# Kernel tuning notes

Hardware: AMD Instinct MI355X
Metric: run time of the kernel (lower is better)

Reference implementation:

```python
import jax, jax.numpy as jnp
import numpy as np

B, T, D = 2, 2048, 2048
Q_HEADS, KV_HEADS, HEAD_DIM = 16, 4, 128
ROPE_BASE = 10000.0


def _apply_rotary(x_nhd, positions_n):
    # x_nhd: (N, H, head_dim); half-split rotary embedding.
    half = x_nhd.shape[-1] // 2
    inv_freq = 1.0 / (ROPE_BASE ** (jnp.arange(half, dtype=jnp.float32) / half))
    ang = positions_n.astype(jnp.float32)[:, None] * inv_freq  # (N, half)
    cos = jnp.cos(ang)[:, None, :]  # (N, 1, half)
    sin = jnp.sin(ang)[:, None, :]
    x1, x2 = x_nhd[..., :half], x_nhd[..., half:]
    return jnp.concatenate([x1 * cos - x2 * sin, x1 * sin + x2 * cos], axis=-1)


def setup_inputs() -> dict:
    key = jax.random.key(0)
    ks = jax.random.split(key, 5)
    s_in = 1.0 / np.sqrt(D)
    s_o = 1.0 / np.sqrt(Q_HEADS * HEAD_DIM)
    x = jax.random.normal(ks[0], (B, T, D), dtype=jnp.float32)
    positions = jnp.broadcast_to(jnp.arange(T, dtype=jnp.int32), (B, T))
    wq = jax.random.normal(ks[1], (Q_HEADS * HEAD_DIM, D), dtype=jnp.float32) * s_in
    wk = jax.random.normal(ks[2], (KV_HEADS * HEAD_DIM, D), dtype=jnp.float32) * s_in
    wv = jax.random.normal(ks[3], (KV_HEADS * HEAD_DIM, D), dtype=jnp.float32) * s_in
    wo = jax.random.normal(ks[4], (D, Q_HEADS * HEAD_DIM), dtype=jnp.float32) * s_o
    return {"x": x, "positions": positions, "wq": wq, "wk": wk, "wv": wv, "wo": wo}


def reference(x, positions, wq, wk, wv, wo):
    bsz, tsz, _ = x.shape
    q = jnp.einsum('btd,od->bto', x, wq).reshape(bsz, tsz, Q_HEADS, HEAD_DIM)
    k = jnp.einsum('btd,od->bto', x, wk).reshape(bsz, tsz, KV_HEADS, HEAD_DIM)
    v = jnp.einsum('btd,od->bto', x, wv).reshape(bsz, tsz, KV_HEADS, HEAD_DIM)
    pos_flat = positions.reshape(-1)
    q = _apply_rotary(q.reshape(-1, Q_HEADS, HEAD_DIM), pos_flat).reshape(bsz, tsz, Q_HEADS, HEAD_DIM)
    k = _apply_rotary(k.reshape(-1, KV_HEADS, HEAD_DIM), pos_flat).reshape(bsz, tsz, KV_HEADS, HEAD_DIM)
    rep = Q_HEADS // KV_HEADS
    k = jnp.repeat(k, rep, axis=2)
    v = jnp.repeat(v, rep, axis=2)
    logits = jnp.einsum('bthd,bThd->bhtT', q, k) / jnp.sqrt(jnp.float32(HEAD_DIM))
    causal = jnp.tril(jnp.ones((tsz, tsz), dtype=bool))
    logits = jnp.where(causal[None, None], logits, -1e9)
    weights = jax.nn.softmax(logits, axis=-1)
    ctx = jnp.einsum('bhtT,bThd->bthd', weights, v).reshape(bsz, tsz, Q_HEADS * HEAD_DIM)
    return jnp.einsum('bto,do->btd', ctx, wo)
```

## Files before the change

### kernel.cpp

```cpp
#include <hip/hip_runtime.h>
#include <hip/hip_bf16.h>

typedef __bf16 bf16x8 __attribute__((ext_vector_type(8)));
typedef float  f32x4  __attribute__((ext_vector_type(4)));
typedef float  f32x16 __attribute__((ext_vector_type(16)));
typedef unsigned int u32x2 __attribute__((ext_vector_type(2)));

#define B_   2
#define T_   2048
#define D_   2048
#define QH_  16
#define KVH_ 4
#define HD_  128
#define BT_  (B_ * T_)
#define KVD_ 512
#define SCL  0.12751744f
#define NIF  -0.20762050593f

#define GLOAD_LDS16(g, l)                                        \
  __builtin_amdgcn_global_load_lds(                              \
      (const __attribute__((address_space(1))) void*)(g),        \
      (__attribute__((address_space(3))) void*)(l), 16, 0, 0)

#define SWZ(row)  ((((row) >> 3) ^ (row)) & 15)
#define SWZ8(row) ((((row) >> 3) ^ (row)) & 7)
#define SWZ4(row) (((row) >> 1) & 3)

__global__ __launch_bounds__(256) void cvt_all(
    const float* __restrict__ x, const float* __restrict__ wq,
    const float* __restrict__ wk, const float* __restrict__ wv,
    const float* __restrict__ wo, ushort* __restrict__ out) {
  const int i = blockIdx.x * 256 + threadIdx.x;
  int j = i;
  const float* src;
  float mul = 1.f;
  if (j < 2097152) { src = x; }
  else if ((j -= 2097152) < 1048576) { src = wq; mul = SCL; }
  else if ((j -= 1048576) < 262144)  { src = wk; }
  else if ((j -= 262144) < 262144)   { src = wv; }
  else { j -= 262144; src = wo; }
  float4 v = ((const float4*)src)[j];
  __hip_bfloat16 h0 = __float2bfloat16(v.x * mul);
  __hip_bfloat16 h1 = __float2bfloat16(v.y * mul);
  __hip_bfloat16 h2 = __float2bfloat16(v.z * mul);
  __hip_bfloat16 h3 = __float2bfloat16(v.w * mul);
  ushort4 o;
  o.x = *(ushort*)&h0; o.y = *(ushort*)&h1;
  o.z = *(ushort*)&h2; o.w = *(ushort*)&h3;
  ((ushort4*)out)[i] = o;
}

__global__ __launch_bounds__(256, 2) void gemm_qkv(
    const ushort* __restrict__ X, const ushort* __restrict__ WQ,
    const ushort* __restrict__ WK, const ushort* __restrict__ WV,
    const int* __restrict__ positions,
    ushort* __restrict__ qo, ushort* __restrict__ ko, ushort* __restrict__ vo) {
  const int nb = blockIdx.x % 24;
  const int mb = blockIdx.x / 24;
  const int tid = threadIdx.x;
  const int wave = tid >> 6;
  const int lane = tid & 63;
  const int mrow = lane & 15;
  const int quad = lane >> 4;
  const int wm = wave >> 1;
  const int wn = wave & 1;
  const int m0 = mb * 128;
  const int K = D_;

  const ushort* Wg;
  if (nb < 16)      Wg = WQ + (size_t)nb * 128 * K;
  else if (nb < 20) Wg = WK + (size_t)(nb - 16) * 128 * K;
  else              Wg = WV + (size_t)(nb - 20) * 128 * K;

  __shared__ __align__(16) ushort smem[16640];
  ushort* Atp = smem;
  ushort* Btp = smem + 8192;

  f32x4 acc[4][4];
#pragma unroll
  for (int i = 0; i < 4; ++i)
#pragma unroll
    for (int j = 0; j < 4; ++j) acc[i][j] = (f32x4){0.f, 0.f, 0.f, 0.f};

  const ushort* Xg = X + (size_t)m0 * K;

  auto STAGE = [&](int buf, int k0) {
#pragma unroll
    for (int p = 0; p < 2; ++p) {
      const int c = p * 256 + tid;
      const int row = c >> 2;
      const int cc = (c & 3) ^ SWZ4(row);
      GLOAD_LDS16(Xg + (size_t)row * K + k0 + cc * 8,
                  Atp + (size_t)buf * 4096 + (size_t)(p * 256 + wave * 64) * 8);
      GLOAD_LDS16(Wg + (size_t)row * K + k0 + cc * 8,
                  Btp + (size_t)buf * 4096 + (size_t)(p * 256 + wave * 64) * 8);
    }
  };

  const int NT = K / 32;
  STAGE(0, 0);
  STAGE(1, 32);

  for (int t = 0; t < NT; ++t) {
    const int cur = t & 1;
    if (t + 2 < NT) asm volatile("s_waitcnt vmcnt(4)" ::: "memory");
    else            asm volatile("s_waitcnt vmcnt(0)" ::: "memory");
    __builtin_amdgcn_s_barrier();

    const ushort* Ac = Atp + (size_t)cur * 4096;
    const ushort* Bc = Btp + (size_t)cur * 4096;
    bf16x8 af[4], bfr[4];
#pragma unroll
    for (int mt = 0; mt < 4; ++mt) {
      const int row = wm * 64 + mt * 16 + mrow;
      af[mt] = *reinterpret_cast<const bf16x8*>(
          Ac + row * 32 + ((quad ^ SWZ4(row)) * 8));
    }
#pragma unroll
    for (int nt = 0; nt < 4; ++nt) {
      const int row = wn * 64 + nt * 16 + mrow;
      bfr[nt] = *reinterpret_cast<const bf16x8*>(
          Bc + row * 32 + ((quad ^ SWZ4(row)) * 8));
    }
#pragma unroll
    for (int mt = 0; mt < 4; ++mt)
#pragma unroll
      for (int nt = 0; nt < 4; ++nt)
        acc[mt][nt] = __builtin_amdgcn_mfma_f32_16x16x32_bf16(
            af[mt], bfr[nt], acc[mt][nt], 0, 0, 0);

    asm volatile("s_waitcnt lgkmcnt(0)" ::: "memory");
    __builtin_amdgcn_s_barrier();
    if (t + 2 < NT) STAGE(cur, (t + 2) * 32);
  }

  if (nb < 20) {
    float* sC = (float*)smem;
    ushort* outp; int ldo, colbase;
    if (nb < 16) { outp = qo; ldo = 2048; colbase = nb * 128; }
    else         { outp = ko; ldo = KVD_; colbase = (nb - 16) * 128; }

    const int col = tid & 63;
    const int wv = tid >> 6;
    const float inv = exp2f((float)col * NIF);

#pragma unroll
    for (int rh = 0; rh < 2; ++rh) {
      if (wm == rh) {
#pragma unroll
        for (int mt = 0; mt < 4; ++mt)
#pragma unroll
          for (int nt = 0; nt < 4; ++nt) {
            const int colw = wn * 64 + nt * 16 + mrow;
            const int r0 = mt * 16 + quad * 4;
#pragma unroll
            for (int r = 0; r < 4; ++r)
              sC[(r0 + r) * 130 + colw] = acc[mt][nt][r];
          }
      }
      __syncthreads();
#pragma unroll 4
      for (int i = 0; i < 16; ++i) {
        const int rl = i * 4 + wv;
        const int grow = m0 + rh * 64 + rl;
        const float x1 = sC[rl * 130 + col];
        const float x2 = sC[rl * 130 + col + 64];
        const float pos = (float)positions[grow];
        const float ang = pos * inv;
        const float cc = cosf(ang);
        const float ss = sinf(ang);
        __hip_bfloat16 h1 = __float2bfloat16(x1 * cc - x2 * ss);
        __hip_bfloat16 h2 = __float2bfloat16(x1 * ss + x2 * cc);
        outp[(size_t)grow * ldo + colbase + col] = *(ushort*)&h1;
        outp[(size_t)grow * ldo + colbase + col + 64] = *(ushort*)&h2;
      }
      __syncthreads();
    }
  } else {
#pragma unroll
    for (int mt = 0; mt < 4; ++mt) {
#pragma unroll
      for (int nt = 0; nt < 4; ++nt) {
        const int colw = wn * 64 + nt * 16 + mrow;
        const int row0 = m0 + wm * 64 + mt * 16 + quad * 4;
        const int col = (nb - 20) * 128 + colw;
        const int bb = row0 >> 11;
        const int t0 = row0 & (T_ - 1);
        ushort4 s4;
#pragma unroll
        for (int r = 0; r < 4; ++r) {
          __hip_bfloat16 hh = __float2bfloat16(acc[mt][nt][r]);
          (&s4.x)[r] = *(ushort*)&hh;
        }
        *(ushort4*)(vo + ((size_t)(bb * KVD_ + col)) * T_ + t0) = s4;
      }
    }
  }
}

__global__ __launch_bounds__(256) void gemm_o(
    const ushort* __restrict__ X, const ushort* __restrict__ W,
    float* __restrict__ Y, int M, int N, int K) {
  const int nb128 = N >> 7;
  const int mb = blockIdx.x / nb128;
  const int nb = blockIdx.x % nb128;
  const int tid = threadIdx.x;
  const int wave = tid >> 6;
  const int lane = tid & 63;
  const int mrow = lane & 15;
  const int quad = lane >> 4;
  const int wm = wave >> 1;
  const int wn = wave & 1;
  const int m0 = mb * 128;
  const int n0 = nb * 128;

  __shared__ __align__(16) ushort At[2][128 * 64];
  __shared__ __align__(16) ushort Bt[2][128 * 64];

  f32x4 acc[4][4];
#pragma unroll
  for (int i = 0; i < 4; ++i)
#pragma unroll
    for (int j = 0; j < 4; ++j) acc[i][j] = (f32x4){0.f, 0.f, 0.f, 0.f};

  const ushort* Xg = X + (size_t)m0 * K;
  const ushort* Wg = W + (size_t)n0 * K;

  auto STAGE = [&](int buf, int k0) {
#pragma unroll
    for (int p = 0; p < 4; ++p) {
      const int c = p * 256 + tid;
      const int row = c >> 3;
      const int cc = (c & 7) ^ (row & 7);
      GLOAD_LDS16(Xg + (size_t)row * K + k0 + cc * 8,
                  At[buf] + (size_t)(p * 256 + wave * 64) * 8);
      GLOAD_LDS16(Wg + (size_t)row * K + k0 + cc * 8,
                  Bt[buf] + (size_t)(p * 256 + wave * 64) * 8);
    }
  };

  const int NT = K / 64;
  STAGE(0, 0);
  STAGE(1, 64);

  for (int t = 0; t < NT; ++t) {
    const int cur = t & 1;
    if (t + 2 < NT) asm volatile("s_waitcnt vmcnt(8)" ::: "memory");
    else            asm volatile("s_waitcnt vmcnt(0)" ::: "memory");
    __builtin_amdgcn_s_barrier();

    const ushort* Ac = At[cur];
    const ushort* Bc = Bt[cur];
#pragma unroll
    for (int s = 0; s < 2; ++s) {
      bf16x8 af[4], bfr[4];
#pragma unroll
      for (int mt = 0; mt < 4; ++mt) {
        const int row = wm * 64 + mt * 16 + mrow;
        af[mt] = *reinterpret_cast<const bf16x8*>(
            Ac + row * 64 + (((s * 4 + quad) ^ (row & 7)) * 8));
      }
#pragma unroll
      for (int nt = 0; nt < 4; ++nt) {
        const int row = wn * 64 + nt * 16 + mrow;
        bfr[nt] = *reinterpret_cast<const bf16x8*>(
            Bc + row * 64 + (((s * 4 + quad) ^ (row & 7)) * 8));
      }
#pragma unroll
      for (int mt = 0; mt < 4; ++mt)
#pragma unroll
        for (int nt = 0; nt < 4; ++nt)
          acc[mt][nt] = __builtin_amdgcn_mfma_f32_16x16x32_bf16(
              af[mt], bfr[nt], acc[mt][nt], 0, 0, 0);
    }

    asm volatile("s_waitcnt lgkmcnt(0)" ::: "memory");
    __builtin_amdgcn_s_barrier();
    if (t + 2 < NT) STAGE(cur, (t + 2) * 64);
  }

#pragma unroll
  for (int mt = 0; mt < 4; ++mt)
#pragma unroll
    for (int nt = 0; nt < 4; ++nt) {
      const int col = n0 + wn * 64 + nt * 16 + mrow;
      const int row0 = m0 + wm * 64 + mt * 16 + quad * 4;
#pragma unroll
      for (int r = 0; r < 4; ++r)
        Y[(size_t)(row0 + r) * N + col] = acc[mt][nt][r];
    }
}

static __device__ __forceinline__ unsigned pk2(float a, float b) {
  __hip_bfloat16 ha = __float2bfloat16(a);
  __hip_bfloat16 hb = __float2bfloat16(b);
  return (unsigned)(*(ushort*)&ha) | ((unsigned)(*(ushort*)&hb) << 16);
}

static __device__ __forceinline__ void hswap(unsigned& a, unsigned& b,
                                             const int hi) {
#if __has_builtin(__builtin_amdgcn_permlane32_swap)
  u32x2 r = __builtin_amdgcn_permlane32_swap(a, b, false, false);
  a = r.x;
  b = r.y;
#else
  unsigned s = __shfl_xor(hi ? a : b, 32, 64);
  unsigned na = hi ? s : a;
  b = hi ? b : s;
  a = na;
#endif
}

__global__ __launch_bounds__(256, 2) void attn_mfma(
    const ushort* __restrict__ q, const ushort* __restrict__ k,
    const ushort* __restrict__ vt, ushort* __restrict__ ctx) {
  const int tid = threadIdx.x;
  const int wave = tid >> 6;
  const int lane = tid & 63;
  const int m5 = lane & 31;
  const int hi = lane >> 5;
  const int parity = wave & 1;
  const int hh = wave >> 1;

  const int pj = blockIdx.x & 31;
  const int g  = blockIdx.x >> 5;
  const int b   = g >> 3;
  const int hkv = (g >> 1) & 3;
  const int hp  = g & 1;
  const int hq  = hkv * 4 + hp * 2 + hh;

  __shared__ __align__(16) ushort smem[32768];
  __shared__ float lbuf[2][32];

  const ushort* kbase = k + ((size_t)b * T_ * KVH_ + hkv) * HD_;
  const ushort* vbase = vt + (size_t)(b * KVD_ + hkv * HD_) * T_;

  for (int job = 0; job < 2; ++job) {
    const int qt = job ? pj : 63 - pj;
    const int q0 = qt * 32;
    const int ns = (qt >> 1) + 1;

    const ushort* qrow =
        q + ((size_t)(b * T_ + q0 + m5) * QH_ + hq) * HD_ + hi * 8;
    bf16x8 qf[8];
#pragma unroll
    for (int c = 0; c < 8; ++c)
      qf[c] = *reinterpret_cast<const bf16x8*>(qrow + c * 16);

    f32x16 o4[4];
#pragma unroll
    for (int dt = 0; dt < 4; ++dt)
#pragma unroll
      for (int r = 0; r < 16; ++r) o4[dt][r] = 0.f;
    float ls = 0.f;

    auto STAGE = [&](int buf, int s) {
      const int j0 = s * 64;
      ushort* kb_ = smem + buf * 16384;
      ushort* vb_ = smem + buf * 16384 + 8192;
#pragma unroll
      for (int p = 0; p < 4; ++p) {
        const int c = p * 256 + tid;
        const int krow = c >> 4;
        const int kco = (c & 15) ^ SWZ(krow);
        GLOAD_LDS16(kbase + (size_t)(j0 + krow) * KVD_ + kco * 8,
                    kb_ + (size_t)(p * 256 + wave * 64) * 8);
      }
#pragma unroll
      for (int p = 0; p < 4; ++p) {
        const int c = p * 256 + tid;
        const int vrow = c >> 3;
        const int vco = (c & 7) ^ SWZ8(vrow);
        GLOAD_LDS16(vbase + (size_t)vrow * T_ + j0 + vco * 8,
                    vb_ + (size_t)(p * 256 + wave * 64) * 8);
      }
    };

    STAGE(0, 0);

    for (int s = 0; s < ns; ++s) {
      const int cur = s & 1;
      if (s + 1 < ns) {
        STAGE(cur ^ 1, s + 1);
        asm volatile("s_waitcnt vmcnt(8)" ::: "memory");
      } else {
        asm volatile("s_waitcnt vmcnt(0)" ::: "memory");
      }
      __builtin_amdgcn_s_barrier();

      const ushort* kt  = smem + cur * 16384;
      const ushort* vtl = smem + cur * 16384 + 8192;
      const int c32 = 2 * s + parity;

      if (c32 <= qt) {
        __builtin_amdgcn_s_setprio(1);
        f32x16 sa;
#pragma unroll
        for (int r = 0; r < 16; ++r) sa[r] = 0.f;
        const int rowk = parity * 32 + m5;
#pragma unroll
        for (int c = 0; c < 8; ++c) {
          const int ch = (2 * c + hi) ^ SWZ(rowk);
          bf16x8 kf =
              *reinterpret_cast<const bf16x8*>(kt + rowk * 128 + ch * 8);
          sa = __builtin_amdgcn_mfma_f32_32x32x16_bf16(kf, qf[c], sa, 0, 0, 0);
        }

        float p[16];
        if (c32 == qt) {
#pragma unroll
          for (int r = 0; r < 16; ++r) {
            const int roff = (r & 3) + 8 * (r >> 2) + 4 * hi;
            p[r] = (roff > m5) ? 0.f : exp2f(sa[r]);
          }
        } else {
#pragma unroll
          for (int r = 0; r < 16; ++r) p[r] = exp2f(sa[r]);
        }
#pragma unroll
        for (int r = 0; r < 16; ++r) ls += p[r];

        unsigned u0 = pk2(p[0], p[1]);   unsigned u1 = pk2(p[2], p[3]);
        unsigned u2 = pk2(p[4], p[5]);   unsigned u3 = pk2(p[6], p[7]);
        unsigned u4 = pk2(p[8], p[9]);   unsigned u5 = pk2(p[10], p[11]);
        unsigned u6 = pk2(p[12], p[13]); unsigned u7 = pk2(p[14], p[15]);
        hswap(u0, u2, hi); hswap(u1, u3, hi);
        hswap(u4, u6, hi); hswap(u5, u7, hi);

#pragma unroll
        for (int half = 0; half < 2; ++half) {
          union { unsigned w[4]; bf16x8 v; } pa;
          pa.w[0] = half ? u4 : u0;
          pa.w[1] = half ? u5 : u1;
          pa.w[2] = half ? u6 : u2;
          pa.w[3] = half ? u7 : u3;
          const int gc2 = parity * 4 + half * 2;
#pragma unroll
          for (int dt = 0; dt < 4; ++dt) {
            const int rowv = dt * 32 + m5;
            const int chv = (gc2 + hi) ^ SWZ8(rowv);
            bf16x8 vf =
                *reinterpret_cast<const bf16x8*>(vtl + rowv * 64 + chv * 8);
            o4[dt] = __builtin_amdgcn_mfma_f32_32x32x16_bf16(pa.v, vf, o4[dt],
                                                             0, 0, 0);
          }
        }
        __builtin_amdgcn_s_setprio(0);
      }

      asm volatile("s_waitcnt lgkmcnt(0)" ::: "memory");
      __builtin_amdgcn_s_barrier();
    }

    const float lt = ls + __shfl_xor(ls, 32, 64);
    float* sO = (float*)smem;
    if (parity) {
#pragma unroll
      for (int reg = 0; reg < 16; ++reg) {
        const int qrw = (reg & 3) + 8 * (reg >> 2) + 4 * hi;
#pragma unroll
        for (int dt = 0; dt < 4; ++dt)
          sO[hh * 4096 + qrw * 128 + dt * 32 + m5] = o4[dt][reg];
      }
      if (hi == 0) lbuf[hh][m5] = lt;
    }
    __syncthreads();
    if (!parity) {
      const float ltot = lt + lbuf[hh][m5];
#pragma unroll
      for (int reg = 0; reg < 16; ++reg) {
        const int qrw = (reg & 3) + 8 * (reg >> 2) + 4 * hi;
        const float rl = 1.f / __shfl(ltot, qrw, 64);
        ushort* op =
            ctx + ((size_t)(b * T_ + q0 + qrw) * QH_ + hq) * HD_ + m5;
#pragma unroll
        for (int dt = 0; dt < 4; ++dt) {
          const float ov =
              o4[dt][reg] + sO[hh * 4096 + qrw * 128 + dt * 32 + m5];
          __hip_bfloat16 hb = __float2bfloat16(ov * rl);
          op[dt * 32] = *(ushort*)&hb;
        }
      }
    }
    __syncthreads();
  }
}

extern "C" void kernel_launch(void* const* d_in, const int* in_sizes, int n_in,
                              void* d_out, int out_size, void* d_ws, size_t ws_size,
                              hipStream_t stream) {
  const float* x  = (const float*)d_in[0];
  const int* pos  = (const int*)d_in[1];
  const float* wq = (const float*)d_in[2];
  const float* wk = (const float*)d_in[3];
  const float* wv = (const float*)d_in[4];
  const float* wo = (const float*)d_in[5];

  ushort* xb  = (ushort*)d_ws;
  ushort* wqb = xb  + (size_t)8388608;
  ushort* wkb = wqb + (size_t)4194304;
  ushort* wvb = wkb + (size_t)1048576;
  ushort* wob = wvb + (size_t)1048576;
  ushort* qb  = wob + (size_t)4194304;
  ushort* kb  = qb  + (size_t)8388608;
  ushort* vtb = kb  + (size_t)2097152;
  ushort* ctx = xb;

  cvt_all<<<18432, 256, 0, stream>>>(x, wq, wk, wv, wo, (ushort*)d_ws);

  gemm_qkv<<<(BT_ / 128) * 24, 256, 0, stream>>>(
      xb, wqb, wkb, wvb, pos, qb, kb, vtb);

  attn_mfma<<<512, 256, 0, stream>>>(qb, kb, vtb, ctx);

  gemm_o<<<(BT_ / 128) * (D_ / 128), 256, 0, stream>>>(
      ctx, wob, (float*)d_out, BT_, D_, QH_ * HD_);
}
```

Baseline: 290.0 us.

## Deepen QKV GEMM K-tile to 64 with single-buffered A and remap gemm_o blocks

The QKV projection GEMM now stages 64-wide K slices with an 8-way XOR swizzle, halving the number of barrier-separated main-loop iterations. X tiles are single-buffered while weight tiles stay double-buffered, and the vmcnt accounting is adjusted to match. The min-blocks launch bound is dropped and LDS grows to 48KB, which may lower occupancy. gemm_o blocks are remapped so that consecutive block IDs spread row tiles across groups of eight, aiming at better L2 locality per XCD; this mapping hard-codes the 32x16 tile grid.

```diff
diff --git a/kernel.cpp b/kernel.cpp
--- a/kernel.cpp
+++ b/kernel.cpp
@@ -24,7 +24,6 @@
 
 #define SWZ(row)  ((((row) >> 3) ^ (row)) & 15)
 #define SWZ8(row) ((((row) >> 3) ^ (row)) & 7)
-#define SWZ4(row) (((row) >> 1) & 3)
 
 __global__ __launch_bounds__(256) void cvt_all(
     const float* __restrict__ x, const float* __restrict__ wq,
@@ -50,7 +49,7 @@
   ((ushort4*)out)[i] = o;
 }
 
-__global__ __launch_bounds__(256, 2) void gemm_qkv(
+__global__ __launch_bounds__(256) void gemm_qkv(
     const ushort* __restrict__ X, const ushort* __restrict__ WQ,
     const ushort* __restrict__ WK, const ushort* __restrict__ WV,
     const int* __restrict__ positions,
@@ -72,9 +71,9 @@
   else if (nb < 20) Wg = WK + (size_t)(nb - 16) * 128 * K;
   else              Wg = WV + (size_t)(nb - 20) * 128 * K;
 
-  __shared__ __align__(16) ushort smem[16640];
-  ushort* Atp = smem;
-  ushort* Btp = smem + 8192;
+  __shared__ __align__(16) ushort smem[24576];
+  ushort* Ab = smem;
+  ushort* Bb = smem + 8192;
 
   f32x4 acc[4][4];
 #pragma unroll
@@ -84,54 +83,67 @@
 
   const ushort* Xg = X + (size_t)m0 * K;
 
-  auto STAGE = [&](int buf, int k0) {
-#pragma unroll
-    for (int p = 0; p < 2; ++p) {
+  auto STAGE_A = [&](int k0) {
+#pragma unroll
+    for (int p = 0; p < 4; ++p) {
       const int c = p * 256 + tid;
-      const int row = c >> 2;
-      const int cc = (c & 3) ^ SWZ4(row);
+      const int row = c >> 3;
+      const int cc = (c & 7) ^ (row & 7);
       GLOAD_LDS16(Xg + (size_t)row * K + k0 + cc * 8,
-                  Atp + (size_t)buf * 4096 + (size_t)(p * 256 + wave * 64) * 8);
+                  Ab + (size_t)(p * 256 + wave * 64) * 8);
+    }
+  };
+  auto STAGE_B = [&](int buf, int k0) {
+#pragma unroll
+    for (int p = 0; p < 4; ++p) {
+      const int c = p * 256 + tid;
+      const int row = c >> 3;
+      const int cc = (c & 7) ^ (row & 7);
       GLOAD_LDS16(Wg + (size_t)row * K + k0 + cc * 8,
-                  Btp + (size_t)buf * 4096 + (size_t)(p * 256 + wave * 64) * 8);
+                  Bb + (size_t)buf * 8192 + (size_t)(p * 256 + wave * 64) * 8);
     }
   };
 
-  const int NT = K / 32;
-  STAGE(0, 0);
-  STAGE(1, 32);
+  const int NT = K / 64;
+  STAGE_A(0);
+  STAGE_B(0, 0);
+  STAGE_B(1, 64);
 
   for (int t = 0; t < NT; ++t) {
     const int cur = t & 1;
-    if (t + 2 < NT) asm volatile("s_waitcnt vmcnt(4)" ::: "memory");
+    if (t + 1 < NT) asm volatile("s_waitcnt vmcnt(4)" ::: "memory");
     else            asm volatile("s_waitcnt vmcnt(0)" ::: "memory");
     __builtin_amdgcn_s_barrier();
 
-    const ushort* Ac = Atp + (size_t)cur * 4096;
-    const ushort* Bc = Btp + (size_t)cur * 4096;
-    bf16x8 af[4], bfr[4];
-#pragma unroll
-    for (int mt = 0; mt < 4; ++mt) {
-      const int row = wm * 64 + mt * 16 + mrow;
-      af[mt] = *reinterpret_cast<const bf16x8*>(
-          Ac + row * 32 + ((quad ^ SWZ4(row)) * 8));
-    }
-#pragma unroll
-    for (int nt = 0; nt < 4; ++nt) {
-      const int row = wn * 64 + nt * 16 + mrow;
-      bfr[nt] = *reinterpret_cast<const bf16x8*>(
-          Bc + row * 32 + ((quad ^ SWZ4(row)) * 8));
-    }
-#pragma unroll
-    for (int mt = 0; mt < 4; ++mt)
-#pragma unroll
-      for (int nt = 0; nt < 4; ++nt)
-        acc[mt][nt] = __builtin_amdgcn_mfma_f32_16x16x32_bf16(
-            af[mt], bfr[nt], acc[mt][nt], 0, 0, 0);
+    const ushort* Ac = Ab;
+    const ushort* Bc = Bb + (size_t)cur * 8192;
+#pragma unroll
+    for (int s = 0; s < 2; ++s) {
+      bf16x8 af[4], bfr[4];
+#pragma unroll
+      for (int mt = 0; mt < 4; ++mt) {
+        const int row = wm * 64 + mt * 16 + mrow;
+        af[mt] = *reinterpret_cast<const bf16x8*>(
+            Ac + row * 64 + (((s * 4 + quad) ^ (row & 7)) * 8));
+      }
+#pragma unroll
+      for (int nt = 0; nt < 4; ++nt) {
+        const int row = wn * 64 + nt * 16 + mrow;
+        bfr[nt] = *reinterpret_cast<const bf16x8*>(
+            Bc + row * 64 + (((s * 4 + quad) ^ (row & 7)) * 8));
+      }
+#pragma unroll
+      for (int mt = 0; mt < 4; ++mt)
+#pragma unroll
+        for (int nt = 0; nt < 4; ++nt)
+          acc[mt][nt] = __builtin_amdgcn_mfma_f32_16x16x32_bf16(
+              af[mt], bfr[nt], acc[mt][nt], 0, 0, 0);
+    }
 
     asm volatile("s_waitcnt lgkmcnt(0)" ::: "memory");
     __builtin_amdgcn_s_barrier();
-    if (t + 2 < NT) STAGE(cur, (t + 2) * 32);
+    if (t + 1 < NT) STAGE_A((t + 1) * 64);
+    if (t + 2 < NT) STAGE_B(cur, (t + 2) * 64);
   }
 
   if (nb < 20) {
@@ -146,6 +158,7 @@
 
 #pragma unroll
     for (int rh = 0; rh < 2; ++rh) {
+      __syncthreads();
       if (wm == rh) {
 #pragma unroll
         for (int mt = 0; mt < 4; ++mt)
@@ -174,7 +187,6 @@
         outp[(size_t)grow * ldo + colbase + col] = *(ushort*)&h1;
         outp[(size_t)grow * ldo + colbase + col + 64] = *(ushort*)&h2;
       }
-      __syncthreads();
     }
   } else {
 #pragma unroll
@@ -201,9 +213,10 @@
 __global__ __launch_bounds__(256) void gemm_o(
     const ushort* __restrict__ X, const ushort* __restrict__ W,
     float* __restrict__ Y, int M, int N, int K) {
-  const int nb128 = N >> 7;
-  const int mb = blockIdx.x / nb128;
-  const int nb = blockIdx.x % nb128;
+  const int bid = blockIdx.x;
+  const int r_  = bid >> 3;
+  const int mb  = (bid & 7) * 4 + (r_ >> 4);
+  const int nb  = r_ & 15;
   const int tid = threadIdx.x;
   const int wave = tid >> 6;
   const int lane = tid & 63;
```

Result: no change. 290.1 us (+0.0%).
